# Kernel optimization log

Measured on AMD Instinct MI355X. Metric: run time of the kernel, lower is better.

Reference implementation:

```python
import jax, jax.numpy as jnp
import numpy as np

NEG_SLOPE = 0.001

def lrelu(x):
    return jnp.where(x >= 0, x, NEG_SLOPE * x)

def conv1x1(w, x):
    # w: [O, C], x: [B, C, H, W] -> [B, O, H, W]
    return jnp.einsum('oc,bchw->bohw', w, x)

def convk(x, w, pad):
    return jax.lax.conv_general_dilated(
        x, w, window_strides=(1, 1), padding=[(pad, pad), (pad, pad)],
        dimension_numbers=('NCHW', 'OIHW', 'NCHW'))

def setup_inputs() -> dict:
    key = jax.random.key(0)
    ks = jax.random.split(key, 15)
    B, C, H, W = 8, 256, 96, 96
    s = 0.05  # weight scale keeps attention logits well-conditioned
    inp = {
        'x':      jax.random.normal(ks[0], (B, C, H, W), jnp.float32),
        'w_f':    jax.random.normal(ks[1], (16, C), jnp.float32) * s,
        'w_beta': jax.random.normal(ks[2], (C, C), jnp.float32) * s,
        'w1':     jax.random.normal(ks[3], (1, 2, 1, 1), jnp.float32) * s,
        'w3':     jax.random.normal(ks[4], (1, 2, 3, 3), jnp.float32) * s,
        'w5':     jax.random.normal(ks[5], (1, 2, 5, 5), jnp.float32) * s,
        'w7':     jax.random.normal(ks[6], (1, 2, 7, 7), jnp.float32) * s,
        'w_a2b':  jax.random.normal(ks[7], (1, C), jnp.float32) * s,
        'w_f2c':  jax.random.normal(ks[8], (1, 4), jnp.float32) * s,
        'w_f2d':  jax.random.normal(ks[9], (C, 4), jnp.float32) * s,
        'w_e':    jax.random.normal(ks[10], (C, C), jnp.float32) * s,
        'w_h':    jax.random.normal(ks[11], (C, 2 * C), jnp.float32) * s,
        'w_m':    jax.random.normal(ks[12], (C, 2 * C), jnp.float32) * s,
        'w_hm':   jax.random.normal(ks[13], (C, 2 * C), jnp.float32) * s,
    }
    return inp

def reference(x, w_f, w_beta, w1, w3, w5, w7, w_a2b, w_f2c, w_f2d, w_e, w_h, w_m, w_hm):
    B, C, H, W = x.shape
    K = w_f.shape[0]  # output2 = 16

    # ---- ChannelAttention ----
    F = conv1x1(w_f, x).reshape(B, K, H * W)          # [B,16,HW]
    A = x.reshape(B, C, H * W)                        # [B,C,HW]
    S = jax.nn.softmax(jnp.einsum('bkn,bcn->bkc', F, A), axis=2)  # softmax over C
    St = jnp.swapaxes(S, 1, 2)                        # [B,C,16]
    E = jnp.einsum('bck,bkn->bcn', St, F).reshape(B, C, H, W)
    out1 = conv1x1(w_beta, E) + x

    # ---- SpatialAttention ----
    avg_out = jnp.mean(x, axis=1, keepdims=True)
    max_out = jnp.max(x, axis=1, keepdims=True)
    AM = jnp.concatenate([avg_out, max_out], axis=1)  # [B,2,H,W]
    S1 = lrelu(convk(AM, w1, 0))
    S3 = lrelu(convk(AM, w3, 1))
    S5 = lrelu(convk(AM, w5, 2))
    S7 = lrelu(convk(AM, w7, 3))
    Bm = lrelu(conv1x1(w_a2b, x))                     # [B,1,H,W]
    F4 = jnp.concatenate([S1, S3, S5, S7], axis=1)    # [B,4,H,W]
    Cm = lrelu(conv1x1(w_f2c, F4))                    # [B,1,H,W]
    D = lrelu(conv1x1(w_f2d, F4))                     # [B,C,H,W]
    B2 = Bm[:, 0]                                     # [B,H,W]
    # torch: C[idx].view([W, H]) is a row-major reshape, NOT a transpose
    C2 = Cm[:, 0].reshape(B, W, H)                    # [B,W,H]
    Ssp = jax.nn.softmax(jnp.einsum('bhw,bwk->bhk', B2, C2), axis=-1)  # [B,H,H]
    Esp = jnp.einsum('bhk,bckw->bchw', Ssp, D)        # [B,C,H,W]
    out2 = conv1x1(w_e, Esp) + x

    # ---- Fusion ----
    out = jnp.concatenate([out1, out2], axis=1)       # [B,2C,H,W]
    Hh = lrelu(conv1x1(w_h, out))
    M = jax.nn.sigmoid(conv1x1(w_m, jnp.concatenate([Hh, x], axis=1)))
    H_M = lrelu(conv1x1(w_hm, jnp.concatenate([Hh, M], axis=1)))
    return H_M
```

## Files before the change

### kernel.cpp

```cpp
#include <hip/hip_runtime.h>

typedef unsigned short u16;
typedef unsigned int   u32;
typedef unsigned long long u64;

#define BN 8
#define CC 256
#define HW 96
#define NN 9216
#define KK 16

typedef __attribute__((ext_vector_type(8))) short bf16x8;
typedef __attribute__((ext_vector_type(4))) float f32x4;

__device__ __forceinline__ float us2f(u16 u){
  union { u32 i; float f; } v; v.i = ((u32)u) << 16; return v.f;
}
__device__ __forceinline__ u16 f2us(float f){
  union { float f; u32 i; } v; v.f = f;
  u32 x = v.i;
  u32 r = (x + 0x7fffu + ((x >> 16) & 1u)) >> 16;
  return (u16)r;
}
__device__ __forceinline__ float lrelu(float v){ return v >= 0.f ? v : 0.001f*v; }

__device__ __forceinline__ u32 swz7(int n, int c){
  return (u32)(n*512 + ((((c>>3) ^ (n&31)) & 31)<<4) + ((c&7)<<1));
}
__device__ __forceinline__ u32 swz8(int col, int k){
  return (u32)(col*256 + ((((k>>3) ^ (col&15)) & 15)<<4) + ((k&7)<<1));
}

__global__ __launch_bounds__(512) void k1_fx(
    const float* __restrict__ x, const float* __restrict__ w_f, const float* __restrict__ w_a2b,
    float* __restrict__ F, float* __restrict__ AM, float* __restrict__ Bm,
    u16* __restrict__ xf, u16* __restrict__ Ff)
{
  __shared__ float wf[CC][KK];
  __shared__ float wa[CC];
  __shared__ float pa[256][KK];
  __shared__ float ps[256], pm[256], pb[256];
  int t = threadIdx.x;
  for (int i = t; i < KK*CC; i += 512) wf[i & 255][i >> 8] = w_f[i];
  if (t < CC) wa[t] = w_a2b[t];
  __syncthreads();
  int half = t >> 8, tp = t & 255;
  int pid = blockIdx.x*256 + tp;
  int b = pid / NN;
  int n = pid % NN;
  const float* xp = x + (size_t)b*CC*NN + n;
  float a0[KK];
  #pragma unroll
  for (int k=0;k<KK;k++) a0[k]=0.f;
  float s0=0.f, m0=-3e38f, b0=0.f;
  int nt = n >> 4, lnn = n & 15;
  u16* xfb = xf + ((size_t)(b*576 + nt)*8)*512;
  int cb0 = half*128;
  #pragma unroll 2
  for (int c8=0; c8<16; ++c8){
    int cb = cb0 + c8*8;
    float v[8];
    #pragma unroll
    for (int e=0;e<8;e++) v[e] = xp[(size_t)(cb+e)*NN];
    union { u16 h[8]; uint4 u; } pk;
    #pragma unroll
    for (int e=0;e<8;e++){
      float vv = v[e];
      s0 += vv;
      m0 = fmaxf(m0, vv);
      b0 = fmaf(wa[cb+e], vv, b0);
      const float* wr = wf[cb+e];
      #pragma unroll
      for (int k=0;k<KK;k++) a0[k] = fmaf(wr[k], vv, a0[k]);
      pk.h[e] = f2us(vv);
    }
    int ks = cb >> 5, lkq = (cb >> 3) & 3;
    *reinterpret_cast<uint4*>(xfb + ((size_t)ks*64 + lkq*16 + lnn)*8) = pk.u;
  }
  if (half){
    #pragma unroll
    for (int k=0;k<KK;k++) pa[tp][k] = a0[k];
    ps[tp] = s0; pm[tp] = m0; pb[tp] = b0;
  }
  __syncthreads();
  if (!half){
    #pragma unroll
    for (int k=0;k<KK;k++) a0[k] += pa[tp][k];
    s0 += ps[tp]; m0 = fmaxf(m0, pm[tp]); b0 += pb[tp];
    float* Fp = F + (size_t)b*KK*NN + n;
    #pragma unroll
    for (int k=0;k<KK;k++) Fp[(size_t)k*NN] = a0[k];
    u16* ffb = Ff + (size_t)(b*576 + nt)*512;
    union { u16 h[8]; uint4 u; } pk2;
    #pragma unroll
    for (int lkq=0; lkq<2; lkq++){
      #pragma unroll
      for (int e=0;e<8;e++) pk2.h[e] = f2us(a0[lkq*8+e]);
      *reinterpret_cast<uint4*>(ffb + ((size_t)lkq*16 + lnn)*8) = pk2.u;
    }
    uint4 z; z.x=z.y=z.z=z.w=0u;
    *reinterpret_cast<uint4*>(ffb + ((size_t)2*16 + lnn)*8) = z;
    *reinterpret_cast<uint4*>(ffb + ((size_t)3*16 + lnn)*8) = z;
    AM[(size_t)b*2*NN + n] = s0*(1.f/256.f);
    AM[(size_t)b*2*NN + NN + n] = m0;
    Bm[(size_t)b*NN + n] = lrelu(b0);
  }
}

__global__ __launch_bounds__(256) void k2_g(
    const float* __restrict__ x, const float* __restrict__ F, float* __restrict__ G)
{
  int b = blockIdx.x >> 6;
  int c0 = (blockIdx.x & 63) * 4;
  int t = threadIdx.x;
  const float* Fp = F + (size_t)b*KK*NN;
  const float* xp = x + ((size_t)b*CC + c0)*NN;
  float acc[KK][4];
  #pragma unroll
  for (int k=0;k<KK;k++){ acc[k][0]=acc[k][1]=acc[k][2]=acc[k][3]=0.f; }
  for (int n = t; n < NN; n += 256){
    float xv0 = xp[n];
    float xv1 = xp[(size_t)NN + n];
    float xv2 = xp[(size_t)2*NN + n];
    float xv3 = xp[(size_t)3*NN + n];
    #pragma unroll
    for (int k=0;k<KK;k++){
      float fv = Fp[(size_t)k*NN + n];
      acc[k][0] = fmaf(fv, xv0, acc[k][0]);
      acc[k][1] = fmaf(fv, xv1, acc[k][1]);
      acc[k][2] = fmaf(fv, xv2, acc[k][2]);
      acc[k][3] = fmaf(fv, xv3, acc[k][3]);
    }
  }
  #pragma unroll
  for (int k=0;k<KK;k++){
    #pragma unroll
    for (int i=0;i<4;i++){
      float v = acc[k][i];
      for (int off=32; off>0; off>>=1) v += __shfl_down(v, off);
      acc[k][i] = v;
    }
  }
  __shared__ float part[4][KK][4];
  int lane = t & 63, wv = t >> 6;
  if (lane == 0){
    #pragma unroll
    for (int k=0;k<KK;k++){ part[wv][k][0]=acc[k][0]; part[wv][k][1]=acc[k][1];
                            part[wv][k][2]=acc[k][2]; part[wv][k][3]=acc[k][3]; }
  }
  __syncthreads();
  if (t < 64){
    int k = t >> 2, i = t & 3;
    float s = part[0][k][i] + part[1][k][i] + part[2][k][i] + part[3][k][i];
    G[((size_t)b*KK + k)*CC + c0 + i] = s;
  }
}

__global__ __launch_bounds__(256) void k3_smws(
    const float* __restrict__ G, const float* __restrict__ w_beta, u16* __restrict__ wspk)
{
  int b = blockIdx.x, t = threadIdx.x;
  __shared__ float sl[KK][CC];
  for (int k=0;k<KK;k++) sl[k][t] = G[((size_t)b*KK + k)*CC + t];
  __syncthreads();
  int lane = t & 63, wv = t >> 6;
  for (int r=0;r<4;r++){
    int k = wv*4 + r;
    float v0 = sl[k][lane], v1 = sl[k][lane+64], v2 = sl[k][lane+128], v3 = sl[k][lane+192];
    float m = fmaxf(fmaxf(v0,v1), fmaxf(v2,v3));
    for (int off=32; off>0; off>>=1) m = fmaxf(m, __shfl_xor(m, off));
    float e0=__expf(v0-m), e1=__expf(v1-m), e2=__expf(v2-m), e3=__expf(v3-m);
    float s = e0+e1+e2+e3;
    for (int off=32; off>0; off>>=1) s += __shfl_xor(s, off);
    float inv = 1.f/s;
    sl[k][lane]=e0*inv; sl[k][lane+64]=e1*inv; sl[k][lane+128]=e2*inv; sl[k][lane+192]=e3*inv;
  }
  __syncthreads();
  const float* wb = w_beta + (size_t)t*CC;
  float acc[KK];
  #pragma unroll
  for (int k=0;k<KK;k++) acc[k]=0.f;
  for (int c=0;c<CC;c++){
    float w = wb[c];
    #pragma unroll
    for (int k=0;k<KK;k++) acc[k] = fmaf(w, sl[k][c], acc[k]);
  }
  int ot = t >> 4, lo = t & 15;
  union { u16 h[8]; uint4 u; } pk;
  #pragma unroll
  for (int lkq=0; lkq<2; lkq++){
    #pragma unroll
    for (int e=0;e<8;e++) pk.h[e] = f2us(acc[lkq*8+e]);
    *reinterpret_cast<uint4*>(wspk + ((size_t)(b*16 + ot)*64 + lkq*16 + lo)*8) = pk.u;
  }
  uint4 z; z.x=z.y=z.z=z.w=0u;
  *reinterpret_cast<uint4*>(wspk + ((size_t)(b*16 + ot)*64 + 2*16 + lo)*8) = z;
  *reinterpret_cast<uint4*>(wspk + ((size_t)(b*16 + ot)*64 + 3*16 + lo)*8) = z;
}

__global__ __launch_bounds__(256) void k5_conv(
    const float* __restrict__ AM, const float* __restrict__ w1, const float* __restrict__ w3,
    const float* __restrict__ w5, const float* __restrict__ w7, const float* __restrict__ wf2c,
    float* __restrict__ F4, float* __restrict__ Cm)
{
  __shared__ float w3l[18], w5l[50], w7l[98], w1l[2], wcl[4];
  int t = threadIdx.x;
  if (t < 2)  w1l[t] = w1[t];
  if (t < 18) w3l[t] = w3[t];
  if (t < 50) w5l[t] = w5[t];
  if (t < 98) w7l[t] = w7[t];
  if (t < 4)  wcl[t] = wf2c[t];
  __syncthreads();
  int gid = blockIdx.x*256 + t;
  int b = gid / NN, n = gid % NN;
  int h = n / HW, w = n % HW;
  const float* am = AM + (size_t)b*2*NN;
  float a0 = am[n], a1 = am[NN + n];
  float s1v = lrelu(a0*w1l[0] + a1*w1l[1]);
  float s3v=0.f, s5v=0.f, s7v=0.f;
  for (int p=-3;p<=3;p++){
    int hh = h + p;
    if (hh < 0 || hh >= HW) continue;
    for (int q=-3;q<=3;q++){
      int ww = w + q;
      if (ww < 0 || ww >= HW) continue;
      float v0 = am[hh*HW+ww], v1 = am[NN + hh*HW + ww];
      s7v += v0*w7l[(p+3)*7 + (q+3)] + v1*w7l[49 + (p+3)*7 + (q+3)];
      if (p>=-2 && p<=2 && q>=-2 && q<=2)
        s5v += v0*w5l[(p+2)*5 + (q+2)] + v1*w5l[25 + (p+2)*5 + (q+2)];
      if (p>=-1 && p<=1 && q>=-1 && q<=1)
        s3v += v0*w3l[(p+1)*3 + (q+1)] + v1*w3l[9 + (p+1)*3 + (q+1)];
    }
  }
  s3v = lrelu(s3v); s5v = lrelu(s5v); s7v = lrelu(s7v);
  float* f4p = F4 + (size_t)b*4*NN + n;
  f4p[0] = s1v; f4p[NN] = s3v; f4p[2*(size_t)NN] = s5v; f4p[3*(size_t)NN] = s7v;
  Cm[(size_t)b*NN + n] = lrelu(s1v*wcl[0] + s3v*wcl[1] + s5v*wcl[2] + s7v*wcl[3]);
}

__global__ __launch_bounds__(256) void k6ab(
    const float* __restrict__ Bm, const float* __restrict__ Cm, u16* __restrict__ spk)
{
  __shared__ float Cl[NN];
  __shared__ float Tl[12][96];
  int t = threadIdx.x;
  int b = blockIdx.x >> 3;
  int hg = blockIdx.x & 7;
  for (int i=t; i<NN/4; i+=256)
    *reinterpret_cast<float4*>(&Cl[i*4]) = *reinterpret_cast<const float4*>(&Cm[(size_t)b*NN + i*4]);
  __syncthreads();
  const float* bp = Bm + (size_t)b*NN + (size_t)hg*12*96;
  for (int g=0; g<2; ++g){
    int idx = g*256 + t;
    if (idx < 288){
      int hr = idx/24, k0 = (idx%24)*4;
      const float* brow = bp + hr*96;
      float a0=0.f,a1=0.f,a2=0.f,a3=0.f;
      for (int w2=0; w2<96; ++w2){
        float bv = brow[w2];
        float4 cv = *reinterpret_cast<const float4*>(&Cl[w2*96 + k0]);
        a0=fmaf(bv,cv.x,a0); a1=fmaf(bv,cv.y,a1); a2=fmaf(bv,cv.z,a2); a3=fmaf(bv,cv.w,a3);
      }
      Tl[hr][k0]=a0; Tl[hr][k0+1]=a1; Tl[hr][k0+2]=a2; Tl[hr][k0+3]=a3;
    }
  }
  __syncthreads();
  if (t < 12){
    int h = hg*12 + t;
    float m = -3e38f;
    for (int k=0;k<96;k++) m = fmaxf(m, Tl[t][k]);
    float s = 0.f;
    for (int k=0;k<96;k++) s += __expf(Tl[t][k]-m);
    float inv = 1.f/s;
    int mf = h >> 4;
    for (int g=0; g<12; g++){
      int ks = g >> 2, lk = g & 3;
      union { u16 hh[8]; uint4 u; } pk;
      #pragma unroll
      for (int e=0;e<8;e++) pk.hh[e] = f2us(__expf(Tl[t][g*8+e]-m)*inv);
      *reinterpret_cast<uint4*>(spk + ((size_t)(((b*6 + mf)*3 + ks)*64) + lk*16 + (h&15))*8) = pk.u;
    }
  }
}

__global__ __launch_bounds__(256) void kw_pack(
    const float* __restrict__ w_h, const float* __restrict__ w_m,
    const float* __restrict__ w_hm, const float* __restrict__ w_e,
    u16* __restrict__ wpk, u16* __restrict__ wpkE)
{
  int gid = blockIdx.x*256 + threadIdx.x;
  if (gid < 49152){
    int mat = gid >> 14;
    int r = gid & 16383;
    int ot = r >> 10;
    int ks = (r >> 6) & 15;
    int l  = r & 63;
    const float* W = (mat==0) ? w_h : ((mat==1) ? w_m : w_hm);
    int o = ot*16 + (l & 15);
    int c = ks*32 + (l >> 4)*8;
    const float* src = W + (size_t)o*512 + c;
    union { u16 h[8]; uint4 u; } pk;
    #pragma unroll
    for (int e=0;e<8;e++) pk.h[e] = f2us(src[e]);
    *reinterpret_cast<uint4*>(wpk + (size_t)gid*8) = pk.u;
  } else {
    int r = gid - 49152;
    int ot = r >> 9;
    int ks = (r >> 6) & 7;
    int l  = r & 63;
    int o = ot*16 + (l & 15);
    int c = ks*32 + (l >> 4)*8;
    const float* src = w_e + (size_t)o*256 + c;
    union { u16 h[8]; uint4 u; } pk;
    #pragma unroll
    for (int e=0;e<8;e++) pk.h[e] = f2us(src[e]);
    *reinterpret_cast<uint4*>(wpkE + (size_t)r*8) = pk.u;
  }
}

__global__ __launch_bounds__(256) void k7m(
    const float* __restrict__ F4, const float* __restrict__ w_f2d,
    const u16* __restrict__ wpkE, u16* __restrict__ WD)
{
  __shared__ uint4 sm4[2048];
  char* sm = reinterpret_cast<char*>(sm4);
  int t = threadIdx.x;
  int b = blockIdx.x / 144;
  int n0 = (blockIdx.x % 144) * 64;
  int n = t & 63, cg = t >> 6;
  float f0 = F4[((size_t)b*4+0)*NN + n0 + n];
  float f1 = F4[((size_t)b*4+1)*NN + n0 + n];
  float f2 = F4[((size_t)b*4+2)*NN + n0 + n];
  float f3 = F4[((size_t)b*4+3)*NN + n0 + n];
  for (int c8 = 0; c8 < 8; ++c8){
    int c = cg*64 + c8*8;
    union { u16 h[8]; uint4 u; } pk;
    #pragma unroll
    for (int e=0;e<8;e++){
      const float* wfp = w_f2d + (size_t)(c+e)*4;
      pk.h[e] = f2us(lrelu(fmaf(wfp[0],f0, fmaf(wfp[1],f1, fmaf(wfp[2],f2, wfp[3]*f3)))));
    }
    *reinterpret_cast<uint4*>(sm + swz7(n, c)) = pk.u;
  }
  __syncthreads();
  int w = t >> 6, l = t & 63, ln = l & 15, lk = l >> 4;
  f32x4 acc[4][4];
  #pragma unroll
  for (int i=0;i<4;i++){ acc[i][0]=0.f; acc[i][1]=0.f; acc[i][2]=0.f; acc[i][3]=0.f; }
  for (int ks=0; ks<8; ++ks){
    bf16x8 bfr[4];
    #pragma unroll
    for (int nf=0; nf<4; nf++)
      bfr[nf] = *reinterpret_cast<const bf16x8*>(sm + swz7(nf*16 + ln, ks*32 + lk*8));
    #pragma unroll
    for (int mf=0; mf<4; mf++){
      bf16x8 afr = *reinterpret_cast<const bf16x8*>(wpkE + ((size_t)((w*4+mf)*8 + ks)*64 + l)*8);
      #pragma unroll
      for (int nf=0; nf<4; nf++)
        acc[mf][nf] = __builtin_amdgcn_mfma_f32_16x16x32_bf16(afr, bfr[nf], acc[mf][nf], 0,0,0);
    }
  }
  #pragma unroll
  for (int mf=0; mf<4; mf++){
    #pragma unroll
    for (int nf=0; nf<4; nf++){
      #pragma unroll
      for (int r=0;r<4;r++){
        int o = (w*4+mf)*16 + lk*4 + r;
        WD[((size_t)b*CC + o)*NN + n0 + nf*16 + ln] = f2us(acc[mf][nf][r]);
      }
    }
  }
}

__global__ __launch_bounds__(256) void k8m(
    const u16* __restrict__ WD, const u16* __restrict__ spk, u16* __restrict__ P)
{
  __shared__ uint4 sm4[3072];
  char* sm = reinterpret_cast<char*>(sm4);
  int t = threadIdx.x;
  int b = blockIdx.x >> 7;
  int o0 = (blockIdx.x & 127) * 2;
  for (int it=0; it<9; ++it){
    int s = it*256 + t;
    int w16 = s % 12;
    int k   = (s / 12) % 96;
    int oi  = s / 1152;
    union { u16 h[8]; uint4 u; } v;
    v.u = *reinterpret_cast<const uint4*>(WD + ((size_t)b*CC + o0+oi)*NN + k*96 + w16*8);
    #pragma unroll
    for (int e=0;e<8;e++){
      int col = oi*96 + w16*8 + e;
      *reinterpret_cast<u16*>(sm + swz8(col, k)) = v.h[e];
    }
  }
  __syncthreads();
  int w = t >> 6, l = t & 63, ln = l & 15, lk = l >> 4;
  f32x4 acc[6][3];
  #pragma unroll
  for (int i=0;i<6;i++){ acc[i][0]=0.f; acc[i][1]=0.f; acc[i][2]=0.f; }
  for (int ks=0; ks<3; ++ks){
    bf16x8 bfr[3];
    #pragma unroll
    for (int j=0;j<3;j++){
      int col = (w*3 + j)*16 + ln;
      bfr[j] = *reinterpret_cast<const bf16x8*>(sm + swz8(col, ks*32 + lk*8));
    }
    #pragma unroll
    for (int mf=0; mf<6; mf++){
      bf16x8 afr = *reinterpret_cast<const bf16x8*>(spk + ((size_t)(((b*6 + mf)*3 + ks)*64) + l)*8);
      #pragma unroll
      for (int j=0;j<3;j++)
        acc[mf][j] = __builtin_amdgcn_mfma_f32_16x16x32_bf16(afr, bfr[j], acc[mf][j], 0,0,0);
    }
  }
  #pragma unroll
  for (int j=0;j<3;j++){
    int col = (w*3 + j)*16 + ln;
    int oi = (col >= 96) ? 1 : 0;
    int ww = col - 96*oi;
    u16* op = P + ((size_t)b*CC + o0+oi)*NN + ww;
    #pragma unroll
    for (int mf=0; mf<6; mf++){
      #pragma unroll
      for (int r=0;r<4;r++){
        int h = mf*16 + lk*4 + r;
        op[(size_t)h*96] = f2us(acc[mf][j][r]);
      }
    }
  }
}

#define TP 72
__global__ __launch_bounds__(256) void k8t(
    const u16* __restrict__ P, const u16* __restrict__ xf, u16* __restrict__ o2t)
{
  __shared__ u16 tl[256*TP];
  int t = threadIdx.x;
  int b = blockIdx.x / 144;
  int tile = blockIdx.x % 144;
  int n0 = tile * 64;
  for (int it=0; it<8; ++it){
    int o = it*32 + (t >> 3);
    int nb = t & 7;
    uint4 v = *reinterpret_cast<const uint4*>(P + ((size_t)b*CC + o)*NN + n0 + nb*8);
    *reinterpret_cast<uint4*>(&tl[o*TP + nb*8]) = v;
  }
  __syncthreads();
  for (int it=0; it<8; ++it){
    int g = it*256 + t;
    int nt_loc = g >> 9;
    int ks = (g >> 6) & 7;
    int lane = g & 63;
    int lkq = lane >> 4, lnn = lane & 15;
    int ob = ks*32 + lkq*8;
    int n_loc = nt_loc*16 + lnn;
    union { u16 h[8]; uint4 u; } gr;
    #pragma unroll
    for (int e=0;e<8;e++) gr.h[e] = tl[(ob+e)*TP + n_loc];
    size_t fo = (((size_t)(b*576 + tile*4 + nt_loc)*8 + ks)*64 + lkq*16 + lnn)*8;
    uint4 xv = *reinterpret_cast<const uint4*>(xf + fo);
    const u32* xp2 = reinterpret_cast<const u32*>(&xv);
    union { u16 h[8]; uint4 u; } res;
    #pragma unroll
    for (int q=0;q<4;q++){
      u32 xw = xp2[q];
      res.h[2*q+0] = f2us(us2f(gr.h[2*q+0]) + us2f((u16)(xw & 0xffffu)));
      res.h[2*q+1] = f2us(us2f(gr.h[2*q+1]) + us2f((u16)(xw >> 16)));
    }
    *reinterpret_cast<uint4*>(o2t + fo) = res.u;
  }
}

__global__ __launch_bounds__(512) void k910(
    const u16* __restrict__ o2t, const u16* __restrict__ xf,
    const u16* __restrict__ Ff, const u16* __restrict__ wspk,
    const u16* __restrict__ wpkH, const u16* __restrict__ wpkM,
    const u16* __restrict__ wpkHM, float* __restrict__ out)
{
  __shared__ uint4 sm4[4096];
  char* sm = reinterpret_cast<char*>(sm4);
  int t = threadIdx.x;
  int b = blockIdx.x / 144;
  int tile = blockIdx.x % 144;
  int n0 = tile * 64;
  int w = t >> 6, l = t & 63, ln = l & 15, lk = l >> 4;
  {
    bf16x8 fb[4];
    #pragma unroll
    for (int nf=0; nf<4; nf++)
      fb[nf] = *reinterpret_cast<const bf16x8*>(Ff + (size_t)(b*576 + tile*4 + nf)*512 + (size_t)l*8);
    #pragma unroll
    for (int mf=0; mf<2; mf++){
      bf16x8 afr = *reinterpret_cast<const bf16x8*>(wspk + ((size_t)(b*16 + w*2 + mf)*64 + l)*8);
      int obase = w*32 + mf*16 + lk*4;
      #pragma unroll
      for (int nf=0; nf<4; nf++){
        f32x4 zz = {0.f,0.f,0.f,0.f};
        f32x4 a1 = __builtin_amdgcn_mfma_f32_16x16x32_bf16(afr, fb[nf], zz, 0,0,0);
        int n = nf*16 + ln;
        int nt = tile*4 + nf;
        u64 xv4 = *reinterpret_cast<const u64*>(
            xf + (((size_t)(b*576 + nt)*8 + (obase>>5))*64 + ((obase>>3)&3)*16 + ln)*8 + (obase&7));
        union { u16 h[4]; u64 u; } pk;
        #pragma unroll
        for (int r=0;r<4;r++)
          pk.h[r] = f2us(a1[r] + us2f((u16)(xv4 >> (16*r))));
        *reinterpret_cast<u64*>(sm + 32768 + swz7(n, obase)) = pk.u;
      }
    }
  }
  __syncthreads();
  f32x4 acc[2][4];
  #pragma unroll
  for (int i=0;i<2;i++){ acc[i][0]=0.f; acc[i][1]=0.f; acc[i][2]=0.f; acc[i][3]=0.f; }
  #pragma unroll 2
  for (int ks=0; ks<16; ++ks){
    bf16x8 bfr[4];
    if (ks < 8){
      int c = ks*32 + lk*8;
      #pragma unroll
      for (int nf=0; nf<4; nf++)
        bfr[nf] = *reinterpret_cast<const bf16x8*>(sm + 32768 + swz7(nf*16 + ln, c));
    } else {
      #pragma unroll
      for (int nf=0; nf<4; nf++)
        bfr[nf] = *reinterpret_cast<const bf16x8*>(o2t + (((size_t)(b*576 + tile*4 + nf)*8 + (ks-8))*64 + l)*8);
    }
    #pragma unroll
    for (int mf=0; mf<2; mf++){
      bf16x8 afr = *reinterpret_cast<const bf16x8*>(wpkH + ((size_t)((w*2+mf)*16 + ks)*64 + l)*8);
      #pragma unroll
      for (int nf=0; nf<4; nf++)
        acc[mf][nf] = __builtin_amdgcn_mfma_f32_16x16x32_bf16(afr, bfr[nf], acc[mf][nf], 0,0,0);
    }
  }
  __syncthreads();
  #pragma unroll
  for (int mf=0; mf<2; mf++){
    int obase = w*32 + mf*16 + lk*4;
    #pragma unroll
    for (int nf=0; nf<4; nf++){
      int n = nf*16 + ln;
      union { u16 h[4]; u64 u; } pk;
      #pragma unroll
      for (int r=0;r<4;r++) pk.h[r] = f2us(lrelu(acc[mf][nf][r]));
      *reinterpret_cast<u64*>(sm + 32768 + swz7(n, obase)) = pk.u;
    }
  }
  __syncthreads();
  #pragma unroll
  for (int i=0;i<2;i++){ acc[i][0]=0.f; acc[i][1]=0.f; acc[i][2]=0.f; acc[i][3]=0.f; }
  #pragma unroll 2
  for (int ks=0; ks<16; ++ks){
    bf16x8 bfr[4];
    if (ks < 8){
      int c = ks*32 + lk*8;
      #pragma unroll
      for (int nf=0; nf<4; nf++)
        bfr[nf] = *reinterpret_cast<const bf16x8*>(sm + 32768 + swz7(nf*16 + ln, c));
    } else {
      #pragma unroll
      for (int nf=0; nf<4; nf++)
        bfr[nf] = *reinterpret_cast<const bf16x8*>(xf + (((size_t)(b*576 + tile*4 + nf)*8 + (ks-8))*64 + l)*8);
    }
    #pragma unroll
    for (int mf=0; mf<2; mf++){
      bf16x8 afr = *reinterpret_cast<const bf16x8*>(wpkM + ((size_t)((w*2+mf)*16 + ks)*64 + l)*8);
      #pragma unroll
      for (int nf=0; nf<4; nf++)
        acc[mf][nf] = __builtin_amdgcn_mfma_f32_16x16x32_bf16(afr, bfr[nf], acc[mf][nf], 0,0,0);
    }
  }
  #pragma unroll
  for (int mf=0; mf<2; mf++){
    int obase = w*32 + mf*16 + lk*4;
    #pragma unroll
    for (int nf=0; nf<4; nf++){
      int n = nf*16 + ln;
      union { u16 h[4]; u64 u; } pk;
      #pragma unroll
      for (int r=0;r<4;r++) pk.h[r] = f2us(1.f/(1.f + __expf(-acc[mf][nf][r])));
      *reinterpret_cast<u64*>(sm + swz7(n, obase)) = pk.u;
    }
  }
  __syncthreads();
  #pragma unroll
  for (int i=0;i<2;i++){ acc[i][0]=0.f; acc[i][1]=0.f; acc[i][2]=0.f; acc[i][3]=0.f; }
  #pragma unroll 2
  for (int ks=0; ks<16; ++ks){
    int c = (ks & 7)*32 + lk*8;
    int roff = (ks < 8) ? 32768 : 0;
    bf16x8 bfr[4];
    #pragma unroll
    for (int nf=0; nf<4; nf++)
      bfr[nf] = *reinterpret_cast<const bf16x8*>(sm + roff + swz7(nf*16 + ln, c));
    #pragma unroll
    for (int mf=0; mf<2; mf++){
      bf16x8 afr = *reinterpret_cast<const bf16x8*>(wpkHM + ((size_t)((w*2+mf)*16 + ks)*64 + l)*8);
      #pragma unroll
      for (int nf=0; nf<4; nf++)
        acc[mf][nf] = __builtin_amdgcn_mfma_f32_16x16x32_bf16(afr, bfr[nf], acc[mf][nf], 0,0,0);
    }
  }
  #pragma unroll
  for (int mf=0; mf<2; mf++){
    #pragma unroll
    for (int nf=0; nf<4; nf++){
      #pragma unroll
      for (int r=0;r<4;r++){
        int o = w*32 + mf*16 + lk*4 + r;
        out[((size_t)b*CC + o)*NN + n0 + nf*16 + ln] = lrelu(acc[mf][nf][r]);
      }
    }
  }
}

extern "C" void kernel_launch(void* const* d_in, const int* in_sizes, int n_in,
                              void* d_out, int out_size, void* d_ws, size_t ws_size,
                              hipStream_t stream)
{
  const float* x     = (const float*)d_in[0];
  const float* w_f   = (const float*)d_in[1];
  const float* w_beta= (const float*)d_in[2];
  const float* w1    = (const float*)d_in[3];
  const float* w3    = (const float*)d_in[4];
  const float* w5    = (const float*)d_in[5];
  const float* w7    = (const float*)d_in[6];
  const float* w_a2b = (const float*)d_in[7];
  const float* w_f2c = (const float*)d_in[8];
  const float* w_f2d = (const float*)d_in[9];
  const float* w_e   = (const float*)d_in[10];
  const float* w_h   = (const float*)d_in[11];
  const float* w_m   = (const float*)d_in[12];
  const float* w_hm  = (const float*)d_in[13];

  char* ws = (char*)d_ws;
  size_t off = 0;
  auto alloc = [&](size_t bytes) -> void* {
    void* p = ws + off; off += (bytes + 255) & ~(size_t)255; return p;
  };
  float* F    = (float*)alloc(sizeof(float)*(size_t)BN*KK*NN);
  float* AMb  = (float*)alloc(sizeof(float)*(size_t)BN*2*NN);
  float* Bmv  = (float*)alloc(sizeof(float)*(size_t)BN*NN);
  float* Cmv  = (float*)alloc(sizeof(float)*(size_t)BN*NN);
  float* F4   = (float*)alloc(sizeof(float)*(size_t)BN*4*NN);
  float* G    = (float*)alloc(sizeof(float)*(size_t)BN*KK*CC);
  u16*   spk  = (u16*)alloc(sizeof(u16)*(size_t)BN*NN);
  u16*   WD   = (u16*)alloc(sizeof(u16)*(size_t)BN*CC*NN);
  u16*   Pm   = (u16*)alloc(sizeof(u16)*(size_t)BN*CC*NN);
  u16*   o2t  = (u16*)alloc(sizeof(u16)*(size_t)BN*CC*NN);
  u16*   xf   = (u16*)alloc(sizeof(u16)*(size_t)BN*CC*NN);
  u16*   Ff   = (u16*)alloc(sizeof(u16)*(size_t)BN*576*512);
  u16*   wpk  = (u16*)alloc(sizeof(u16)*(size_t)3*16384*8);
  u16*   wpkE = (u16*)alloc(sizeof(u16)*(size_t)8192*8);
  u16*   wspk = (u16*)alloc(sizeof(u16)*(size_t)BN*16*64*8);
  (void)ws_size; (void)in_sizes; (void)n_in; (void)out_size;

  u16* wpkH  = wpk;
  u16* wpkM  = wpk + (size_t)16384*8;
  u16* wpkHM = wpk + (size_t)2*16384*8;

  kw_pack <<<224, 256, 0, stream>>>(w_h, w_m, w_hm, w_e, wpk, wpkE);
  k1_fx   <<<288, 512, 0, stream>>>(x, w_f, w_a2b, F, AMb, Bmv, xf, Ff);
  k2_g    <<<512, 256, 0, stream>>>(x, F, G);
  k3_smws <<<8,   256, 0, stream>>>(G, w_beta, wspk);
  k5_conv <<<288, 256, 0, stream>>>(AMb, w1, w3, w5, w7, w_f2c, F4, Cmv);
  k6ab    <<<64,  256, 0, stream>>>(Bmv, Cmv, spk);
  k7m     <<<1152,256, 0, stream>>>(F4, w_f2d, wpkE, WD);
  k8m     <<<1024,256, 0, stream>>>(WD, spk, Pm);
  k8t     <<<1152,256, 0, stream>>>(Pm, xf, o2t);
  k910    <<<1152,512, 0, stream>>>(o2t, xf, Ff, wspk, wpkH, wpkM, wpkHM, (float*)d_out);
}
```

Measured before the change: 281.7 us.

## Fuse spatial-attention matmul with residual add and fragment-layout transpose

Merges the k8m matmul (Ssp × D) with the k8t transpose-plus-residual kernel. The new kernel retiles blocks to 8 output channels by 16 columns and writes results straight into the MFMA fragment layout, adding xf inline. This removes the intermediate Pm buffer and one full read and write of a B×C×N bf16 tensor, plus a kernel launch. In exchange the output stores are scattered 2-byte writes and the xf loads are unvectorized, which may hurt memory coalescing.

```diff
diff --git a/kernel.cpp b/kernel.cpp
--- a/kernel.cpp
+++ b/kernel.cpp
@@ -373,102 +373,64 @@
   }
 }
 
-__global__ __launch_bounds__(256) void k8m(
-    const u16* __restrict__ WD, const u16* __restrict__ spk, u16* __restrict__ P)
-{
-  __shared__ uint4 sm4[3072];
-  char* sm = reinterpret_cast<char*>(sm4);
+__global__ __launch_bounds__(256) void k8v2(
+    const u16* __restrict__ WD, const u16* __restrict__ spk,
+    const u16* __restrict__ xf, u16* __restrict__ o2t)
+{
+  __shared__ char sm[32768];
   int t = threadIdx.x;
-  int b = blockIdx.x >> 7;
-  int o0 = (blockIdx.x & 127) * 2;
-  for (int it=0; it<9; ++it){
+  int bi = blockIdx.x;
+  int b  = bi / 192;
+  int rem = bi % 192;
+  int ws = rem / 32;
+  int og = rem % 32;
+  for (int it=0; it<6; ++it){
     int s = it*256 + t;
-    int w16 = s % 12;
-    int k   = (s / 12) % 96;
-    int oi  = s / 1152;
+    int wq = s & 1;
+    int k  = (s >> 1) % 96;
+    int o  = s / 192;
     union { u16 h[8]; uint4 u; } v;
-    v.u = *reinterpret_cast<const uint4*>(WD + ((size_t)b*CC + o0+oi)*NN + k*96 + w16*8);
+    v.u = *reinterpret_cast<const uint4*>(WD + ((size_t)b*CC + og*8 + o)*NN + k*96 + ws*16 + wq*8);
     #pragma unroll
     for (int e=0;e<8;e++){
-      int col = oi*96 + w16*8 + e;
+      int col = (wq*8+e)*8 + o;
       *reinterpret_cast<u16*>(sm + swz8(col, k)) = v.h[e];
     }
   }
   __syncthreads();
   int w = t >> 6, l = t & 63, ln = l & 15, lk = l >> 4;
-  f32x4 acc[6][3];
-  #pragma unroll
-  for (int i=0;i<6;i++){ acc[i][0]=0.f; acc[i][1]=0.f; acc[i][2]=0.f; }
+  f32x4 acc[6][2];
+  #pragma unroll
+  for (int i=0;i<6;i++){ acc[i][0]=0.f; acc[i][1]=0.f; }
   for (int ks=0; ks<3; ++ks){
-    bf16x8 bfr[3];
-    #pragma unroll
-    for (int j=0;j<3;j++){
-      int col = (w*3 + j)*16 + ln;
+    bf16x8 bfr[2];
+    #pragma unroll
+    for (int j=0;j<2;j++){
+      int col = (w*2 + j)*16 + ln;
       bfr[j] = *reinterpret_cast<const bf16x8*>(sm + swz8(col, ks*32 + lk*8));
     }
     #pragma unroll
     for (int mf=0; mf<6; mf++){
       bf16x8 afr = *reinterpret_cast<const bf16x8*>(spk + ((size_t)(((b*6 + mf)*3 + ks)*64) + l)*8);
       #pragma unroll
-      for (int j=0;j<3;j++)
+      for (int j=0;j<2;j++)
         acc[mf][j] = __builtin_amdgcn_mfma_f32_16x16x32_bf16(afr, bfr[j], acc[mf][j], 0,0,0);
     }
   }
-  #pragma unroll
-  for (int j=0;j<3;j++){
-    int col = (w*3 + j)*16 + ln;
-    int oi = (col >= 96) ? 1 : 0;
-    int ww = col - 96*oi;
-    u16* op = P + ((size_t)b*CC + o0+oi)*NN + ww;
+  int ksg = og >> 2, lkq = og & 3;
+  #pragma unroll
+  for (int j=0;j<2;j++){
+    int col = (w*2 + j)*16 + ln;
+    int wl = col >> 3, ol = col & 7;
     #pragma unroll
     for (int mf=0; mf<6; mf++){
       #pragma unroll
       for (int r=0;r<4;r++){
         int h = mf*16 + lk*4 + r;
-        op[(size_t)h*96] = f2us(acc[mf][j][r]);
+        size_t fo = (((size_t)(b*576 + h*6 + ws)*8 + ksg)*64 + lkq*16 + wl)*8 + ol;
+        o2t[fo] = f2us(acc[mf][j][r] + us2f(xf[fo]));
       }
     }
-  }
-}
-
-#define TP 72
-__global__ __launch_bounds__(256) void k8t(
-    const u16* __restrict__ P, const u16* __restrict__ xf, u16* __restrict__ o2t)
-{
-  __shared__ u16 tl[256*TP];
-  int t = threadIdx.x;
-  int b = blockIdx.x / 144;
-  int tile = blockIdx.x % 144;
-  int n0 = tile * 64;
-  for (int it=0; it<8; ++it){
-    int o = it*32 + (t >> 3);
-    int nb = t & 7;
-    uint4 v = *reinterpret_cast<const uint4*>(P + ((size_t)b*CC + o)*NN + n0 + nb*8);
-    *reinterpret_cast<uint4*>(&tl[o*TP + nb*8]) = v;
-  }
-  __syncthreads();
-  for (int it=0; it<8; ++it){
-    int g = it*256 + t;
-    int nt_loc = g >> 9;
-    int ks = (g >> 6) & 7;
-    int lane = g & 63;
-    int lkq = lane >> 4, lnn = lane & 15;
-    int ob = ks*32 + lkq*8;
-    int n_loc = nt_loc*16 + lnn;
-    union { u16 h[8]; uint4 u; } gr;
-    #pragma unroll
-    for (int e=0;e<8;e++) gr.h[e] = tl[(ob+e)*TP + n_loc];
-    size_t fo = (((size_t)(b*576 + tile*4 + nt_loc)*8 + ks)*64 + lkq*16 + lnn)*8;
-    uint4 xv = *reinterpret_cast<const uint4*>(xf + fo);
-    const u32* xp2 = reinterpret_cast<const u32*>(&xv);
-    union { u16 h[8]; uint4 u; } res;
-    #pragma unroll
-    for (int q=0;q<4;q++){
-      u32 xw = xp2[q];
-      res.h[2*q+0] = f2us(us2f(gr.h[2*q+0]) + us2f((u16)(xw & 0xffffu)));
-      res.h[2*q+1] = f2us(us2f(gr.h[2*q+1]) + us2f((u16)(xw >> 16)));
-    }
-    *reinterpret_cast<uint4*>(o2t + fo) = res.u;
   }
 }
 
@@ -648,7 +610,6 @@
   float* G    = (float*)alloc(sizeof(float)*(size_t)BN*KK*CC);
   u16*   spk  = (u16*)alloc(sizeof(u16)*(size_t)BN*NN);
   u16*   WD   = (u16*)alloc(sizeof(u16)*(size_t)BN*CC*NN);
-  u16*   Pm   = (u16*)alloc(sizeof(u16)*(size_t)BN*CC*NN);
   u16*   o2t  = (u16*)alloc(sizeof(u16)*(size_t)BN*CC*NN);
   u16*   xf   = (u16*)alloc(sizeof(u16)*(size_t)BN*CC*NN);
   u16*   Ff   = (u16*)alloc(sizeof(u16)*(size_t)BN*576*512);
@@ -668,7 +629,6 @@
   k5_conv <<<288, 256, 0, stream>>>(AMb, w1, w3, w5, w7, w_f2c, F4, Cmv);
   k6ab    <<<64,  256, 0, stream>>>(Bmv, Cmv, spk);
   k7m     <<<1152,256, 0, stream>>>(F4, w_f2d, wpkE, WD);
-  k8m     <<<1024,256, 0, stream>>>(WD, spk, Pm);
-  k8t     <<<1152,256, 0, stream>>>(Pm, xf, o2t);
+  k8v2    <<<1536,256, 0, stream>>>(WD, spk, xf, o2t);
   k910    <<<1152,512, 0, stream>>>(o2t, xf, Ff, wspk, wpkH, wpkM, wpkHM, (float*)d_out);
 }
```

New measurement: 286.2 us. No clear change (+1.6%).
